# Kernel tuning notes

Measured on AMD Instinct MI355X. Metric: run time of the kernel, lower is better.

The kernel has to match this reference:

```python
import jax, jax.numpy as jnp
import numpy as np

B, S, H, N = 2, 2048, 1024, 16
D = H // N


def setup_inputs() -> dict:
    key = jax.random.key(0)
    k1, k2, k3 = jax.random.split(key, 3)
    # Xavier-uniform-ish init for projection weights
    lim_in = (6.0 / (H + 3 * H)) ** 0.5
    lim_out = (6.0 / (H + H)) ** 0.5
    return {
        "hidden_states": jax.random.normal(k1, (B, S, H), dtype=jnp.float32),
        "w_in": jax.random.uniform(k2, (3 * H, H), minval=-lim_in, maxval=lim_in, dtype=jnp.float32),
        "b_in": jnp.zeros((3 * H,), dtype=jnp.float32),
        "w_out": jax.random.uniform(k3, (H, H), minval=-lim_out, maxval=lim_out, dtype=jnp.float32),
        "b_out": jnp.zeros((H,), dtype=jnp.float32),
    }


def reference(hidden_states, w_in, b_in, w_out, b_out):
    b, s, h = hidden_states.shape
    qkv = hidden_states @ w_in.T + b_in  # [B,S,3H]
    q, k, v = jnp.split(qkv, 3, axis=-1)
    # [B,S,H] -> [B,N,S,D]
    def to_heads(x):
        return x.reshape(b, s, N, D).transpose(0, 2, 1, 3)
    q, k, v = to_heads(q), to_heads(k), to_heads(v)
    scale = D ** -0.5
    scores = jnp.einsum("bnqd,bnkd->bnqk", q, k) * scale  # [B,N,S,S]
    causal = jnp.triu(jnp.ones((s, s), dtype=bool), k=1)
    scores = jnp.where(causal, -jnp.inf, scores)
    attn = jax.nn.softmax(scores, axis=-1)
    out = jnp.einsum("bnqk,bnkd->bnqd", attn, v)  # [B,N,S,D]
    out = out.transpose(0, 2, 1, 3).reshape(b, s, h)
    return out @ w_out.T + b_out
```

## Files before the change

### kernel.cpp

```cpp
#include <hip/hip_runtime.h>
#include <hip/hip_bf16.h>

#define BB 2
#define SS 2048
#define HH 1024
#define NH 16
#define DD 64
#define H3 3072
#define MM (BB*SS)

typedef unsigned short u16;
typedef unsigned int u32;
typedef __attribute__((ext_vector_type(8))) short bf16x8;
typedef __attribute__((ext_vector_type(4))) float f32x4;

__device__ __forceinline__ u16 f2bf(float f) {
    union { float f; u32 u; } v; v.f = f;
    u32 u = v.u;
    u += 0x7fffu + ((u >> 16) & 1u);
    return (u16)(u >> 16);
}
__device__ __forceinline__ float bf2f(u16 h) {
    union { u32 u; float f; } v; v.u = ((u32)h) << 16;
    return v.f;
}
__device__ __forceinline__ u32 pack2bf(float a, float b) {
    __hip_bfloat162 h = __float22bfloat162_rn(float2{a, b});
    u32 u; __builtin_memcpy(&u, &h, 4);
    return u;
}
__device__ __forceinline__ void gl_lds16(const void* g, void* l) {
    __builtin_amdgcn_global_load_lds(
        (const __attribute__((address_space(1))) u32*)g,
        (__attribute__((address_space(3))) u32*)l, 16, 0, 0);
}

__global__ void cvt3bf(const float4* __restrict__ s0, uint2* __restrict__ d0, int n0,
                       const float4* __restrict__ s1, uint2* __restrict__ d1, int n1,
                       const float4* __restrict__ s2, uint2* __restrict__ d2, int n2) {
    int i = blockIdx.x * blockDim.x + threadIdx.x;
    const int tot = n0 + n1 + n2;
    for (; i < tot; i += gridDim.x * blockDim.x) {
        const float4* s; uint2* d; int j;
        if (i < n0)            { s = s0; d = d0; j = i; }
        else if (i < n0 + n1)  { s = s1; d = d1; j = i - n0; }
        else                   { s = s2; d = d2; j = i - n0 - n1; }
        float4 v = s[j];
        uint2 o; o.x = pack2bf(v.x, v.y); o.y = pack2bf(v.z, v.w);
        d[j] = o;
    }
}

template<int BN, int MODE>
__global__ __launch_bounds__(256, 2)
void gemm_k2(const u16* __restrict__ A, const u16* __restrict__ Bbf,
             const u16* __restrict__ biasbf, void* __restrict__ Cptr,
             u16* __restrict__ Qo, u16* __restrict__ Ko, u16* __restrict__ Vto,
             int M, int Nn, int K)
{
    constexpr int NFR = BN / 32;
    __shared__ __align__(16) u16 Alds[128 * 32];
    __shared__ __align__(16) u16 Blds[BN * 32];
    const int tid = threadIdx.x;
    const int w = tid >> 6, lane = tid & 63, quad = lane >> 4, l16 = lane & 15;
    const int m0 = blockIdx.x * 128, n0 = blockIdx.y * BN;
    const int wm = w >> 1, wn = w & 1;
    const int rA4 = lane >> 2, c8b = (lane & 3) * 8;

    f32x4 acc[4][NFR] = {};

    for (int k0 = 0; k0 < K; k0 += 32) {
        __syncthreads();
#pragma unroll
        for (int q = 0; q < 2; ++q) {
            int row0 = w * 32 + q * 16;
            gl_lds16(&A[(size_t)(m0 + row0 + rA4) * K + k0 + c8b], &Alds[row0 * 32]);
        }
#pragma unroll
        for (int q = 0; q < BN / 64; ++q) {
            int row0 = w * (BN / 4) + q * 16;
            gl_lds16(&Bbf[(size_t)(n0 + row0 + rA4) * K + k0 + c8b], &Blds[row0 * 32]);
        }
        __syncthreads();

        bf16x8 af[4], bfr[NFR];
#pragma unroll
        for (int mi = 0; mi < 4; ++mi)
            af[mi] = *(const bf16x8*)&Alds[(wm * 64 + mi * 16 + l16) * 32 + quad * 8];
#pragma unroll
        for (int ni = 0; ni < NFR; ++ni)
            bfr[ni] = *(const bf16x8*)&Blds[(wn * (BN / 2) + ni * 16 + l16) * 32 + quad * 8];
#pragma unroll
        for (int mi = 0; mi < 4; ++mi)
#pragma unroll
            for (int ni = 0; ni < NFR; ++ni)
                acc[mi][ni] = __builtin_amdgcn_mfma_f32_16x16x32_bf16(
                    af[mi], bfr[ni], acc[mi][ni], 0, 0, 0);
    }

#pragma unroll
    for (int mi = 0; mi < 4; ++mi) {
        int row_b = m0 + wm * 64 + mi * 16 + quad * 4;
#pragma unroll
        for (int ni = 0; ni < NFR; ++ni) {
            int col = n0 + wn * (BN / 2) + ni * 16 + l16;
            float bv = bf2f(biasbf[col]);
            if constexpr (MODE == 1) {
#pragma unroll
                for (int i = 0; i < 4; ++i)
                    ((float*)Cptr)[(size_t)(row_b + i) * Nn + col] = acc[mi][ni][i] + bv;
            } else {
                if (col < 1024) {
#pragma unroll
                    for (int i = 0; i < 4; ++i)
                        Qo[(size_t)(row_b + i) * 1024 + col] =
                            f2bf((acc[mi][ni][i] + bv) * 0.125f);
                } else if (col < 2048) {
#pragma unroll
                    for (int i = 0; i < 4; ++i)
                        Ko[(size_t)(row_b + i) * 1024 + (col - 1024)] =
                            f2bf(acc[mi][ni][i] + bv);
                } else {
                    int d = col - 2048, hh = d >> 6, dd = d & 63;
                    int b = row_b >> 11, s = row_b & 2047;
                    u16 t0 = f2bf(acc[mi][ni][0] + bv), t1 = f2bf(acc[mi][ni][1] + bv);
                    u16 t2 = f2bf(acc[mi][ni][2] + bv), t3 = f2bf(acc[mi][ni][3] + bv);
                    uint2 pk; pk.x = (u32)t0 | ((u32)t1 << 16);
                    pk.y = (u32)t2 | ((u32)t3 << 16);
                    *(uint2*)&Vto[((size_t)((b * 16 + hh) * 64 + dd)) * 2048 + s] = pk;
                }
            }
        }
    }
}

__global__ __launch_bounds__(256, 2)
void attn_v3(const u16* __restrict__ Q, const u16* __restrict__ Kb,
             const u16* __restrict__ Vt, u16* __restrict__ attn_out) {
    const int pr = blockIdx.x, h = blockIdx.y, b = blockIdx.z;
    const int tid = threadIdx.x;
    const int w = tid >> 6, lane = tid & 63, quad = lane >> 4, l16 = lane & 15;
    __shared__ __align__(16) u16 Klds[2][64 * 72];
    __shared__ __align__(16) u16 Vlds[2][64 * 72];
    __shared__ __align__(16) u16 Pb[4][16 * 72];
    const int r0 = tid >> 3, cc8 = (tid & 7) * 8;

    for (int half = 0; half < 2; ++half) {
        const int qt = half ? pr : (31 - pr);
        const int q0 = qt * 64;
        const int T = qt + 1;

        const u16* Qb = Q  + (size_t)(b * SS + q0) * 1024 + h * 64;
        const u16* Kg = Kb + (size_t)(b * SS) * 1024 + h * 64;
        const u16* Vg = Vt + (size_t)((b * 16 + h) * 64) * 2048;

        bf16x8 qf0 = *(const bf16x8*)&Qb[(size_t)(w * 16 + l16) * 1024 + quad * 8];
        bf16x8 qf1 = *(const bf16x8*)&Qb[(size_t)(w * 16 + l16) * 1024 + 32 + quad * 8];

        f32x4 oacc[4] = {};
        float lp[4] = {0.f, 0.f, 0.f, 0.f};

        uint4 kr0 = *(const uint4*)&Kg[(size_t)r0 * 1024 + cc8];
        uint4 kr1 = *(const uint4*)&Kg[(size_t)(r0 + 32) * 1024 + cc8];
        uint4 vr0 = *(const uint4*)&Vg[(size_t)r0 * 2048 + cc8];
        uint4 vr1 = *(const uint4*)&Vg[(size_t)(r0 + 32) * 2048 + cc8];
        __syncthreads();
        *(uint4*)&Klds[0][r0 * 72 + cc8]        = kr0;
        *(uint4*)&Klds[0][(r0 + 32) * 72 + cc8] = kr1;
        *(uint4*)&Vlds[0][r0 * 72 + cc8]        = vr0;
        *(uint4*)&Vlds[0][(r0 + 32) * 72 + cc8] = vr1;

        for (int t = 0; t < T; ++t) {
            const int cur = t & 1;
            __syncthreads();
            if (t + 1 < T) {
                const int nv = (t + 1) * 64;
                kr0 = *(const uint4*)&Kg[(size_t)(nv + r0) * 1024 + cc8];
                kr1 = *(const uint4*)&Kg[(size_t)(nv + r0 + 32) * 1024 + cc8];
                vr0 = *(const uint4*)&Vg[(size_t)r0 * 2048 + nv + cc8];
                vr1 = *(const uint4*)&Vg[(size_t)(r0 + 32) * 2048 + nv + cc8];
            }
            f32x4 sacc[4] = {};
#pragma unroll
            for (int ni = 0; ni < 4; ++ni) {
                bf16x8 kf0 = *(const bf16x8*)&Klds[cur][(ni * 16 + l16) * 72 + quad * 8];
                bf16x8 kf1 = *(const bf16x8*)&Klds[cur][(ni * 16 + l16) * 72 + 32 + quad * 8];
                sacc[ni] = __builtin_amdgcn_mfma_f32_16x16x32_bf16(qf0, kf0, sacc[ni], 0, 0, 0);
                sacc[ni] = __builtin_amdgcn_mfma_f32_16x16x32_bf16(qf1, kf1, sacc[ni], 0, 0, 0);
            }
            const int kv0 = t * 64;
#pragma unroll
            for (int ni = 0; ni < 4; ++ni) {
                int colg = kv0 + ni * 16 + l16;
#pragma unroll
                for (int i = 0; i < 4; ++i) {
                    int rowg = q0 + w * 16 + quad * 4 + i;
                    float p = (colg <= rowg) ? __expf(sacc[ni][i]) : 0.f;
                    lp[i] += p;
                    Pb[w][(quad * 4 + i) * 72 + ni * 16 + l16] = f2bf(p);
                }
            }
            bf16x8 pf0 = *(const bf16x8*)&Pb[w][l16 * 72 + quad * 8];
            bf16x8 pf1 = *(const bf16x8*)&Pb[w][l16 * 72 + 32 + quad * 8];
#pragma unroll
            for (int ni = 0; ni < 4; ++ni) {
                bf16x8 vf0 = *(const bf16x8*)&Vlds[cur][(ni * 16 + l16) * 72 + quad * 8];
                bf16x8 vf1 = *(const bf16x8*)&Vlds[cur][(ni * 16 + l16) * 72 + 32 + quad * 8];
                oacc[ni] = __builtin_amdgcn_mfma_f32_16x16x32_bf16(pf0, vf0, oacc[ni], 0, 0, 0);
                oacc[ni] = __builtin_amdgcn_mfma_f32_16x16x32_bf16(pf1, vf1, oacc[ni], 0, 0, 0);
            }
            if (t + 1 < T) {
                const int nxt = cur ^ 1;
                *(uint4*)&Klds[nxt][r0 * 72 + cc8]        = kr0;
                *(uint4*)&Klds[nxt][(r0 + 32) * 72 + cc8] = kr1;
                *(uint4*)&Vlds[nxt][r0 * 72 + cc8]        = vr0;
                *(uint4*)&Vlds[nxt][(r0 + 32) * 72 + cc8] = vr1;
            }
        }

#pragma unroll
        for (int i = 0; i < 4; ++i) {
#pragma unroll
            for (int s = 1; s < 16; s <<= 1)
                lp[i] += __shfl_xor(lp[i], s, 64);
            lp[i] = 1.0f / lp[i];
        }
        u16* ob = attn_out + (size_t)(b * SS + q0 + w * 16) * 1024 + h * 64;
#pragma unroll
        for (int ni = 0; ni < 4; ++ni)
#pragma unroll
            for (int i = 0; i < 4; ++i)
                ob[(size_t)(quad * 4 + i) * 1024 + ni * 16 + l16] =
                    f2bf(oacc[ni][i] * lp[i]);
    }
}

extern "C" void kernel_launch(void* const* d_in, const int* in_sizes, int n_in,
                              void* d_out, int out_size, void* d_ws, size_t ws_size,
                              hipStream_t stream) {
    const float* hidden = (const float*)d_in[0];
    const float* w_in   = (const float*)d_in[1];
    const float* b_in   = (const float*)d_in[2];
    const float* w_out  = (const float*)d_in[3];
    const float* b_out  = (const float*)d_in[4];
    float* out = (float*)d_out;

    char* ws = (char*)d_ws;
    u16* hid_bf  = (u16*)d_out;
    u16* wi_bf   = (u16*)ws;
    u16* bi_bf   = (u16*)(ws + 6291456);
    u16* attn_ws = (u16*)ws;
    u16* Qbuf    = (u16*)(ws + 8388608);
    u16* wo_bf   = (u16*)(ws + 8388608);
    u16* bo_bf   = (u16*)(ws + 8388608 + 2097152);
    u16* Kbuf    = (u16*)(ws + 16777216);
    u16* Vtbuf   = (u16*)(ws + 25165824);

    cvt3bf<<<dim3(2048), dim3(256), 0, stream>>>(
        (const float4*)hidden, (uint2*)hid_bf, 1048576,
        (const float4*)w_in,   (uint2*)wi_bf,  786432,
        (const float4*)b_in,   (uint2*)bi_bf,  768);
    gemm_k2<128, 2><<<dim3(32, 24), dim3(256), 0, stream>>>(
        hid_bf, wi_bf, bi_bf, nullptr, Qbuf, Kbuf, Vtbuf, MM, H3, HH);
    attn_v3<<<dim3(16, NH, BB), dim3(256), 0, stream>>>(
        Qbuf, Kbuf, Vtbuf, attn_ws);
    cvt3bf<<<dim3(512), dim3(256), 0, stream>>>(
        (const float4*)w_out, (uint2*)wo_bf, 262144,
        (const float4*)b_out, (uint2*)bo_bf, 256,
        nullptr, nullptr, 0);
    gemm_k2<64, 1><<<dim3(32, 16), dim3(256), 0, stream>>>(
        attn_ws, wo_bf, bo_bf, out, nullptr, nullptr, nullptr, MM, HH, HH);
}
```

Baseline: 186.6 us.

## Compute transposed scores so P feeds PV MFMA from registers without LDS

Swaps the MFMA operand order so the score tile comes out transposed, and permutes the K row placement in LDS so each lane's exp'd scores pack directly into the bf16 A-operand of the PV MFMA. This removes the per-wave P staging buffer in shared memory and its writes and reads. The causal mask now runs only on the diagonal tile, and row sums are reduced with fewer shuffles. The risk is correctness of the row permutation and index mapping.

```diff
diff --git a/kernel.cpp b/kernel.cpp
--- a/kernel.cpp
+++ b/kernel.cpp
@@ -135,15 +135,15 @@
 }
 
 __global__ __launch_bounds__(256, 2)
-void attn_v3(const u16* __restrict__ Q, const u16* __restrict__ Kb,
+void attn_v4(const u16* __restrict__ Q, const u16* __restrict__ Kb,
              const u16* __restrict__ Vt, u16* __restrict__ attn_out) {
     const int pr = blockIdx.x, h = blockIdx.y, b = blockIdx.z;
     const int tid = threadIdx.x;
     const int w = tid >> 6, lane = tid & 63, quad = lane >> 4, l16 = lane & 15;
     __shared__ __align__(16) u16 Klds[2][64 * 72];
     __shared__ __align__(16) u16 Vlds[2][64 * 72];
-    __shared__ __align__(16) u16 Pb[4][16 * 72];
     const int r0 = tid >> 3, cc8 = (tid & 7) * 8;
+    const int Rp = ((r0 & 4) << 2) | ((r0 & 24) >> 1) | (r0 & 3);
 
     for (int half = 0; half < 2; ++half) {
         const int qt = half ? pr : (31 - pr);
@@ -158,15 +158,15 @@
         bf16x8 qf1 = *(const bf16x8*)&Qb[(size_t)(w * 16 + l16) * 1024 + 32 + quad * 8];
 
         f32x4 oacc[4] = {};
-        float lp[4] = {0.f, 0.f, 0.f, 0.f};
+        float lp = 0.f;
 
         uint4 kr0 = *(const uint4*)&Kg[(size_t)r0 * 1024 + cc8];
         uint4 kr1 = *(const uint4*)&Kg[(size_t)(r0 + 32) * 1024 + cc8];
         uint4 vr0 = *(const uint4*)&Vg[(size_t)r0 * 2048 + cc8];
         uint4 vr1 = *(const uint4*)&Vg[(size_t)(r0 + 32) * 2048 + cc8];
         __syncthreads();
-        *(uint4*)&Klds[0][r0 * 72 + cc8]        = kr0;
-        *(uint4*)&Klds[0][(r0 + 32) * 72 + cc8] = kr1;
+        *(uint4*)&Klds[0][Rp * 72 + cc8]        = kr0;
+        *(uint4*)&Klds[0][(Rp + 32) * 72 + cc8] = kr1;
         *(uint4*)&Vlds[0][r0 * 72 + cc8]        = vr0;
         *(uint4*)&Vlds[0][(r0 + 32) * 72 + cc8] = vr1;
 
@@ -185,53 +185,70 @@
             for (int ni = 0; ni < 4; ++ni) {
                 bf16x8 kf0 = *(const bf16x8*)&Klds[cur][(ni * 16 + l16) * 72 + quad * 8];
                 bf16x8 kf1 = *(const bf16x8*)&Klds[cur][(ni * 16 + l16) * 72 + 32 + quad * 8];
-                sacc[ni] = __builtin_amdgcn_mfma_f32_16x16x32_bf16(qf0, kf0, sacc[ni], 0, 0, 0);
-                sacc[ni] = __builtin_amdgcn_mfma_f32_16x16x32_bf16(qf1, kf1, sacc[ni], 0, 0, 0);
-            }
-            const int kv0 = t * 64;
-#pragma unroll
-            for (int ni = 0; ni < 4; ++ni) {
-                int colg = kv0 + ni * 16 + l16;
-#pragma unroll
-                for (int i = 0; i < 4; ++i) {
-                    int rowg = q0 + w * 16 + quad * 4 + i;
-                    float p = (colg <= rowg) ? __expf(sacc[ni][i]) : 0.f;
-                    lp[i] += p;
-                    Pb[w][(quad * 4 + i) * 72 + ni * 16 + l16] = f2bf(p);
+                sacc[ni] = __builtin_amdgcn_mfma_f32_16x16x32_bf16(kf0, qf0, sacc[ni], 0, 0, 0);
+                sacc[ni] = __builtin_amdgcn_mfma_f32_16x16x32_bf16(kf1, qf1, sacc[ni], 0, 0, 0);
+            }
+            u32 pk[4][2];
+            if (t + 1 < T) {
+#pragma unroll
+                for (int ni = 0; ni < 4; ++ni) {
+                    float p0 = __expf(sacc[ni][0]), p1 = __expf(sacc[ni][1]);
+                    float p2 = __expf(sacc[ni][2]), p3 = __expf(sacc[ni][3]);
+                    lp += (p0 + p1) + (p2 + p3);
+                    pk[ni][0] = pack2bf(p0, p1);
+                    pk[ni][1] = pack2bf(p2, p3);
                 }
-            }
-            bf16x8 pf0 = *(const bf16x8*)&Pb[w][l16 * 72 + quad * 8];
-            bf16x8 pf1 = *(const bf16x8*)&Pb[w][l16 * 72 + 32 + quad * 8];
+            } else {
+                const int thr = w * 16 + l16;
+#pragma unroll
+                for (int ni = 0; ni < 4; ++ni) {
+                    const int pb = 32 * (ni >> 1) + 8 * quad + 4 * (ni & 1);
+                    float pv[4];
+#pragma unroll
+                    for (int i = 0; i < 4; ++i) {
+                        float e = __expf(sacc[ni][i]);
+                        pv[i] = (pb + i <= thr) ? e : 0.f;
+                    }
+                    lp += (pv[0] + pv[1]) + (pv[2] + pv[3]);
+                    pk[ni][0] = pack2bf(pv[0], pv[1]);
+                    pk[ni][1] = pack2bf(pv[2], pv[3]);
+                }
+            }
+            union { u32 u[4]; bf16x8 v; } pf0, pf1;
+            pf0.u[0] = pk[0][0]; pf0.u[1] = pk[0][1];
+            pf0.u[2] = pk[1][0]; pf0.u[3] = pk[1][1];
+            pf1.u[0] = pk[2][0]; pf1.u[1] = pk[2][1];
+            pf1.u[2] = pk[3][0]; pf1.u[3] = pk[3][1];
 #pragma unroll
             for (int ni = 0; ni < 4; ++ni) {
                 bf16x8 vf0 = *(const bf16x8*)&Vlds[cur][(ni * 16 + l16) * 72 + quad * 8];
                 bf16x8 vf1 = *(const bf16x8*)&Vlds[cur][(ni * 16 + l16) * 72 + 32 + quad * 8];
-                oacc[ni] = __builtin_amdgcn_mfma_f32_16x16x32_bf16(pf0, vf0, oacc[ni], 0, 0, 0);
-                oacc[ni] = __builtin_amdgcn_mfma_f32_16x16x32_bf16(pf1, vf1, oacc[ni], 0, 0, 0);
+                oacc[ni] = __builtin_amdgcn_mfma_f32_16x16x32_bf16(pf0.v, vf0, oacc[ni], 0, 0, 0);
+                oacc[ni] = __builtin_amdgcn_mfma_f32_16x16x32_bf16(pf1.v, vf1, oacc[ni], 0, 0, 0);
             }
             if (t + 1 < T) {
                 const int nxt = cur ^ 1;
-                *(uint4*)&Klds[nxt][r0 * 72 + cc8]        = kr0;
-                *(uint4*)&Klds[nxt][(r0 + 32) * 72 + cc8] = kr1;
+                *(uint4*)&Klds[nxt][Rp * 72 + cc8]        = kr0;
+                *(uint4*)&Klds[nxt][(Rp + 32) * 72 + cc8] = kr1;
                 *(uint4*)&Vlds[nxt][r0 * 72 + cc8]        = vr0;
                 *(uint4*)&Vlds[nxt][(r0 + 32) * 72 + cc8] = vr1;
             }
         }
 
-#pragma unroll
-        for (int i = 0; i < 4; ++i) {
-#pragma unroll
-            for (int s = 1; s < 16; s <<= 1)
-                lp[i] += __shfl_xor(lp[i], s, 64);
-            lp[i] = 1.0f / lp[i];
-        }
+        lp += __shfl_xor(lp, 16, 64);
+        lp += __shfl_xor(lp, 32, 64);
+        float linv[4];
+#pragma unroll
+        for (int i = 0; i < 4; ++i)
+            linv[i] = 1.0f / __shfl(lp, quad * 4 + i, 64);
+
         u16* ob = attn_out + (size_t)(b * SS + q0 + w * 16) * 1024 + h * 64;
 #pragma unroll
         for (int ni = 0; ni < 4; ++ni)
 #pragma unroll
             for (int i = 0; i < 4; ++i)
                 ob[(size_t)(quad * 4 + i) * 1024 + ni * 16 + l16] =
-                    f2bf(oacc[ni][i] * lp[i]);
+                    f2bf(oacc[ni][i] * linv[i]);
     }
 }
 
@@ -262,7 +279,7 @@
         (const float4*)b_in,   (uint2*)bi_bf,  768);
     gemm_k2<128, 2><<<dim3(32, 24), dim3(256), 0, stream>>>(
         hid_bf, wi_bf, bi_bf, nullptr, Qbuf, Kbuf, Vtbuf, MM, H3, HH);
-    attn_v3<<<dim3(16, NH, BB), dim3(256), 0, stream>>>(
+    attn_v4<<<dim3(16, NH, BB), dim3(256), 0, stream>>>(
         Qbuf, Kbuf, Vtbuf, attn_ws);
     cvt3bf<<<dim3(512), dim3(256), 0, stream>>>(
         (const float4*)w_out, (uint2*)wo_bf, 262144,
```

After: 178.9 us. -4.1%, faster.
